# Kernel optimization log

Hardware: AMD Instinct MI355X
Metric: run time of the kernel (lower is better)

The kernel has to match this reference:

```python
import jax, jax.numpy as jnp
import numpy as np

# global prototype index ranges per scale: scale s owns protos [s0, s1)
SCALES = ((0, 100), (100, 200))
NEG = jnp.float32(-1e30)


def _scale_terms(d, lab_flat, cls_of):
    """d: [B,P,Hs,Ws] distances for this scale; lab_flat: [B,N] downsampled labels
    (already shifted by -1); cls_of: [P] class id of each local prototype.
    Returns (sum of exp(-sym_kld) over valid prototype pairs, number of valid pairs).
    """
    B, P = d.shape[0], d.shape[1]
    dflat = d.reshape(B, P, -1)                                   # [B,P,N]
    M = lab_flat[:, None, :] == cls_of[None, :, None]             # [B,P,N] pixel mask per proto's class
    count = M.sum(-1)                                             # [B,P] masked pixel count
    # masked log_softmax over the class pixels of each prototype
    lse = jax.nn.logsumexp(jnp.where(M, dflat, NEG), axis=-1)     # [B,P]
    L = jnp.where(M, dflat - lse[:, :, None], 0.0)                # log-probs on mask, 0 elsewhere
    Pr = jnp.where(M, jnp.exp(L), 0.0)                            # probs on mask, 0 elsewhere
    E = jnp.sum(Pr * L, axis=-1)                                  # [B,P] sum p*log p
    # Cmat[b,a,c] = sum_n Pr[b,a,n] * L[b,c,n]
    Cmat = jnp.einsum('ban,bcn->bac', Pr, L)                      # [B,P,P]
    # sym_kld[b,j,k] = 0.5*((E_k - sum p_k log p_j) + (E_j - sum p_j log p_k))
    kld = 0.5 * (E[:, None, :] + E[:, :, None] - Cmat - jnp.swapaxes(Cmat, 1, 2))
    idx = jnp.arange(P)
    same = (cls_of[:, None] == cls_of[None, :]) & (idx[:, None] < idx[None, :])  # j<k, same class
    valid = same[None] & (count[:, :, None] >= 2) & (count[:, None, :] >= 2)      # need >=2 masked pixels
    return jnp.sum(jnp.where(valid, jnp.exp(-kld), 0.0)), jnp.sum(valid)


def reference(dist0, dist1, target_labels, proto_class):
    lab = target_labels - 1                                       # [B,H,W], -1 = ignore
    B, H, W = lab.shape
    tot = jnp.float32(0.0)
    cnt = jnp.int32(0)
    for d, (s0, s1) in zip((dist0, dist1), SCALES):
        Hs, Ws = d.shape[2], d.shape[3]
        # torch F.interpolate(mode='nearest'): src index = floor(dst * in/out)
        ri = (jnp.arange(Hs) * H) // Hs
        ci = (jnp.arange(Ws) * W) // Ws
        lab_flat = lab[:, ri][:, :, ci].reshape(B, Hs * Ws)
        s, n = _scale_terms(d, lab_flat, proto_class[s0:s1])
        tot = tot + s
        cnt = cnt + n
    return jnp.where(cnt > 0, tot / jnp.maximum(cnt, 1).astype(jnp.float32), jnp.float32(0.0))


def setup_inputs() -> dict:
    key = jax.random.key(0)
    k0, k1, k2 = jax.random.split(key, 3)
    B, C, PPC = 16, 20, 5  # batch, num classes, protos per class per scale
    dist0 = jax.random.normal(k0, (B, 100, 128, 128), dtype=jnp.float32)
    dist1 = jax.random.normal(k1, (B, 100, 64, 64), dtype=jnp.float32)
    # labels in 1..C ; 0 becomes -1 after the shift and is ignored
    target_labels = jax.random.randint(k2, (B, 512, 512), 0, C + 1).astype(jnp.int32)
    proto_class = ((jnp.arange(200) % 100) // PPC).astype(jnp.int32)
    return {"dist0": dist0, "dist1": dist1, "target_labels": target_labels, "proto_class": proto_class}
```

## Files before the change

kernel.cpp:

```cpp
#include <hip/hip_runtime.h>
#include <math.h>

#define TPB 256
#define NCLS 20
#define PPC 5
#define NB 16
#define N0 16384
#define N1 4096
#define SEGCAP 96
#define RECSZ 36
#define NBLKA 1600
#define NBLKB 640

__global__ void downsample_labels(const int* __restrict__ tgt,
                                  char* __restrict__ lab0, char* __restrict__ lab1) {
    const int q = blockIdx.x * blockDim.x + threadIdx.x;
    if (q < 65536) {
        const int b = q >> 12, r = q & 4095;
        const int i = r >> 5, j0 = (r & 31) << 2;
        const int* src = tgt + b * 262144 + (i << 2) * 512;
        char4 v;
        v.x = (char)(src[(j0 + 0) << 2] - 1);
        v.y = (char)(src[(j0 + 1) << 2] - 1);
        v.z = (char)(src[(j0 + 2) << 2] - 1);
        v.w = (char)(src[(j0 + 3) << 2] - 1);
        ((char4*)lab0)[q] = v;
    } else {
        const int k = q - 65536;
        const int b = k >> 10, r = k & 1023;
        const int i = r >> 4, j0 = (r & 15) << 2;
        const int* src = tgt + b * 262144 + (i << 3) * 512;
        char4 v;
        v.x = (char)(src[(j0 + 0) << 3] - 1);
        v.y = (char)(src[(j0 + 1) << 3] - 1);
        v.z = (char)(src[(j0 + 2) << 3] - 1);
        v.w = (char)(src[(j0 + 3) << 3] - 1);
        ((char4*)lab1)[k] = v;
    }
}

__global__ __launch_bounds__(TPB) void kA(const float* __restrict__ dist0,
                                          const float* __restrict__ dist1,
                                          const char* __restrict__ lab0,
                                          const char* __restrict__ lab1,
                                          float* __restrict__ recs) {
    __shared__ float vals[4][PPC][SEGCAP];

    const int blk = blockIdx.x;
    int scale, bc, split;
    if (blk < 1280) { scale = 0; bc = blk >> 2; split = blk & 3; }
    else            { scale = 1; bc = blk - 1280; split = 0; }
    const int b = bc / NCLS, c = bc % NCLS;
    const int N = scale ? N1 : N0;
    const float* dist = scale ? dist1 : dist0;
    const char* lab = (scale ? lab1 + b * N1 : lab0 + b * N0) + split * 4096;

    const float4* rows4[PPC];
#pragma unroll
    for (int p = 0; p < PPC; ++p)
        rows4[p] = (const float4*)(dist + (size_t)(b * 100 + c * PPC + p) * N + split * 4096);
    const char4* lab4 = (const char4*)lab;

    const int tid = threadIdx.x, lane = tid & 63, w = tid >> 6;
    const unsigned long long below = (lane == 63) ? 0x7fffffffffffffffull
                                                  : ((1ull << lane) - 1ull);

    int wK = 0;
#pragma unroll
    for (int it = 0; it < 4; ++it) {
        const int idx4 = w * 256 + it * 64 + lane;
        const char4 lb = lab4[idx4];
        const float4 a0 = rows4[0][idx4], a1 = rows4[1][idx4], a2 = rows4[2][idx4],
                     a3 = rows4[3][idx4], a4 = rows4[4][idx4];
#define DO_E(F)                                                                        \
        { const bool mt = ((int)lb.F == c);                                            \
          const unsigned long long bal = __ballot(mt);                                 \
          if (mt) { const int pos = wK + (int)__popcll(bal & below);                   \
            if (pos < SEGCAP) {                                                        \
              vals[w][0][pos] = a0.F; vals[w][1][pos] = a1.F; vals[w][2][pos] = a2.F;  \
              vals[w][3][pos] = a3.F; vals[w][4][pos] = a4.F; } }                      \
          wK += (int)__popcll(bal); }
        DO_E(x) DO_E(y) DO_E(z) DO_E(w)
#undef DO_E
    }

    float mx[PPC], sm[PPC], T1[PPC * PPC];
#pragma unroll
    for (int p = 0; p < PPC; ++p) { mx[p] = -INFINITY; sm[p] = 0.f; }
#pragma unroll
    for (int i = 0; i < PPC * PPC; ++i) T1[i] = 0.f;

    if (wK <= SEGCAP) {
        for (int k = lane; k < wK; k += 64)
#pragma unroll
            for (int p = 0; p < PPC; ++p) mx[p] = fmaxf(mx[p], vals[w][p][k]);
#pragma unroll
        for (int d = 32; d >= 1; d >>= 1)
#pragma unroll
            for (int p = 0; p < PPC; ++p) mx[p] = fmaxf(mx[p], __shfl_xor(mx[p], d, 64));
        for (int k = lane; k < wK; k += 64) {
            float dv[PPC], ev[PPC];
#pragma unroll
            for (int p = 0; p < PPC; ++p) {
                dv[p] = vals[w][p][k];
                ev[p] = __expf(dv[p] - mx[p]);
                sm[p] += ev[p];
            }
#pragma unroll
            for (int aa = 0; aa < PPC; ++aa)
#pragma unroll
                for (int bb = 0; bb < PPC; ++bb)
                    T1[aa * PPC + bb] = fmaf(ev[aa], dv[bb], T1[aa * PPC + bb]);
        }
    } else {
#pragma unroll
        for (int it = 0; it < 4; ++it) {
            const int idx4 = w * 256 + it * 64 + lane;
            const char4 lb = lab4[idx4];
            const float4 a0 = rows4[0][idx4], a1 = rows4[1][idx4], a2 = rows4[2][idx4],
                         a3 = rows4[3][idx4], a4 = rows4[4][idx4];
#define FB_MAX(F)                                                                      \
            if ((int)lb.F == c) {                                                      \
                mx[0] = fmaxf(mx[0], a0.F); mx[1] = fmaxf(mx[1], a1.F);                \
                mx[2] = fmaxf(mx[2], a2.F); mx[3] = fmaxf(mx[3], a3.F);                \
                mx[4] = fmaxf(mx[4], a4.F); }
            FB_MAX(x) FB_MAX(y) FB_MAX(z) FB_MAX(w)
#undef FB_MAX
        }
#pragma unroll
        for (int d = 32; d >= 1; d >>= 1)
#pragma unroll
            for (int p = 0; p < PPC; ++p) mx[p] = fmaxf(mx[p], __shfl_xor(mx[p], d, 64));
#pragma unroll
        for (int it = 0; it < 4; ++it) {
            const int idx4 = w * 256 + it * 64 + lane;
            const char4 lb = lab4[idx4];
            const float4 a0 = rows4[0][idx4], a1 = rows4[1][idx4], a2 = rows4[2][idx4],
                         a3 = rows4[3][idx4], a4 = rows4[4][idx4];
#define FB_SUM(F)                                                                      \
            if ((int)lb.F == c) {                                                      \
                float dv[PPC] = {a0.F, a1.F, a2.F, a3.F, a4.F};                        \
                float ev[PPC];                                                         \
                _Pragma("unroll")                                                      \
                for (int p = 0; p < PPC; ++p) {                                        \
                    ev[p] = __expf(dv[p] - mx[p]); sm[p] += ev[p]; }                   \
                _Pragma("unroll")                                                      \
                for (int aa = 0; aa < PPC; ++aa)                                       \
                _Pragma("unroll")                                                      \
                    for (int bb = 0; bb < PPC; ++bb)                                   \
                        T1[aa * PPC + bb] = fmaf(ev[aa], dv[bb], T1[aa * PPC + bb]); }
            FB_SUM(x) FB_SUM(y) FB_SUM(z) FB_SUM(w)
#undef FB_SUM
        }
    }

#pragma unroll
    for (int d = 32; d >= 1; d >>= 1) {
#pragma unroll
        for (int p = 0; p < PPC; ++p) sm[p] += __shfl_xor(sm[p], d, 64);
#pragma unroll
        for (int i = 0; i < PPC * PPC; ++i) T1[i] += __shfl_xor(T1[i], d, 64);
    }

    if (lane == 0) {
        float* r = recs + (size_t)(blk * 4 + w) * RECSZ;
#pragma unroll
        for (int p = 0; p < PPC; ++p) { r[p] = mx[p]; r[PPC + p] = sm[p]; }
#pragma unroll
        for (int i = 0; i < PPC * PPC; ++i) r[10 + i] = T1[i];
        r[35] = (float)wK;
    }
}

__global__ __launch_bounds__(64) void kB(const float* __restrict__ recs,
                                         float* __restrict__ psum,
                                         float* __restrict__ pcnt) {
    const int blk = blockIdx.x;
    const int lane = threadIdx.x;
    const int scale = (blk >= 320) ? 1 : 0;
    const int bc = blk - scale * 320;
    const int rbase = scale ? (5120 + bc * 4) : (bc * 16);
    const int nrec = scale ? 4 : 16;
    const int a = (lane < 25) ? lane / 5 : 0;
    const int bb = (lane < 25) ? lane % 5 : 0;

    float M = -INFINITY, cnt = 0.f;
    if (lane < 5)
        for (int r = 0; r < nrec; ++r)
            M = fmaxf(M, recs[(size_t)(rbase + r) * RECSZ + lane]);
    if (lane == 0)
        for (int r = 0; r < nrec; ++r)
            cnt += recs[(size_t)(rbase + r) * RECSZ + 35];
    cnt = __shfl(cnt, 0, 64);

    float S = 0.f;
    if (lane < 5)
        for (int r = 0; r < nrec; ++r) {
            const float* rr = recs + (size_t)(rbase + r) * RECSZ;
            S += rr[5 + lane] * expf(rr[lane] - M);
        }
    float lse = 0.f;
    if (lane < 5) lse = M + logf(S);

    const float Ma    = __shfl(M, a, 64);
    const float Sa    = __shfl(S, a, 64);
    const float lse_b = __shfl(lse, bb, 64);

    float U = 0.f;
    if (lane < 25)
        for (int r = 0; r < nrec; ++r) {
            const float* rr = recs + (size_t)(rbase + r) * RECSZ;
            U += rr[10 + lane] * expf(rr[a] - Ma);
        }
    const float C = U / Sa - lse_b;

    float tot = 0.f;
#pragma unroll
    for (int j = 0; j < PPC; ++j)
#pragma unroll
        for (int k = j + 1; k < PPC; ++k) {
            const float Ejj = __shfl(C, j * 5 + j, 64);
            const float Ekk = __shfl(C, k * 5 + k, 64);
            const float Cjk = __shfl(C, j * 5 + k, 64);
            const float Ckj = __shfl(C, k * 5 + j, 64);
            tot += expf(-0.5f * (Ejj + Ekk - Cjk - Ckj));
        }
    if (lane == 0) {
        const bool ok = (cnt >= 2.f);
        psum[blk] = ok ? tot : 0.f;
        pcnt[blk] = ok ? 10.f : 0.f;
    }
}

__global__ void finalize_kernel(const float* __restrict__ psum,
                                const float* __restrict__ pcnt,
                                float* __restrict__ out) {
    __shared__ float rs[TPB], rc[TPB];
    const int tid = threadIdx.x;
    float s = 0.f, c = 0.f;
    for (int i = tid; i < NBLKB; i += TPB) { s += psum[i]; c += pcnt[i]; }
    rs[tid] = s; rc[tid] = c;
    __syncthreads();
    for (int off = 128; off > 0; off >>= 1) {
        if (tid < off) { rs[tid] += rs[tid + off]; rc[tid] += rc[tid + off]; }
        __syncthreads();
    }
    if (tid == 0) out[0] = (rc[0] > 0.f) ? (rs[0] / rc[0]) : 0.f;
}

extern "C" void kernel_launch(void* const* d_in, const int* in_sizes, int n_in,
                              void* d_out, int out_size, void* d_ws, size_t ws_size,
                              hipStream_t stream) {
    const float* dist0 = (const float*)d_in[0];
    const float* dist1 = (const float*)d_in[1];
    const int*   tgt   = (const int*)d_in[2];
    float* out = (float*)d_out;

    char*  lab0 = (char*)d_ws;
    char*  lab1 = lab0 + 262144;
    float* recs = (float*)(lab0 + 327680);
    float* psum = recs + (size_t)NBLKA * 4 * RECSZ;
    float* pcnt = psum + NBLKB;

    downsample_labels<<<320, TPB, 0, stream>>>(tgt, lab0, lab1);
    kA<<<NBLKA, TPB, 0, stream>>>(dist0, dist1, lab0, lab1, recs);
    kB<<<NBLKB, 64, 0, stream>>>(recs, psum, pcnt);
    finalize_kernel<<<1, TPB, 0, stream>>>(psum, pcnt, out);
}
```

Before: 50.22 us.

## Replace LDS compaction with per-lane online softmax accumulation in kA

Removes the ballot-based compaction into shared memory and the two-pass max/sum (plus the global-reload fallback). Each lane now keeps an online max-rescaled running softmax sum and a 5x5 cross-term matrix over its own masked pixels. The lanes are then merged with a wave-wide max and rescale before the shuffle reductions. All loads are issued up front into registers, and launch bounds request 2 blocks per CU. This trades LDS traffic and the divergent fallback for more exps per masked pixel, heavy register use (80 float4 plus 25 accumulators), and divergent per-lane branches.

```diff
diff --git a/kernel.cpp b/kernel.cpp
--- a/kernel.cpp
+++ b/kernel.cpp
@@ -7,7 +7,6 @@
 #define NB 16
 #define N0 16384
 #define N1 4096
-#define SEGCAP 96
 #define RECSZ 36
 #define NBLKA 1600
 #define NBLKB 640
@@ -39,13 +38,11 @@
     }
 }
 
-__global__ __launch_bounds__(TPB) void kA(const float* __restrict__ dist0,
-                                          const float* __restrict__ dist1,
-                                          const char* __restrict__ lab0,
-                                          const char* __restrict__ lab1,
-                                          float* __restrict__ recs) {
-    __shared__ float vals[4][PPC][SEGCAP];
-
+__global__ __launch_bounds__(TPB, 2) void kA(const float* __restrict__ dist0,
+                                             const float* __restrict__ dist1,
+                                             const char* __restrict__ lab0,
+                                             const char* __restrict__ lab1,
+                                             float* __restrict__ recs) {
     const int blk = blockIdx.x;
     int scale, bc, split;
     if (blk < 1280) { scale = 0; bc = blk >> 2; split = blk & 3; }
@@ -55,120 +52,83 @@
     const float* dist = scale ? dist1 : dist0;
     const char* lab = (scale ? lab1 + b * N1 : lab0 + b * N0) + split * 4096;
 
-    const float4* rows4[PPC];
-#pragma unroll
-    for (int p = 0; p < PPC; ++p)
-        rows4[p] = (const float4*)(dist + (size_t)(b * 100 + c * PPC + p) * N + split * 4096);
+    const int tid = threadIdx.x, lane = tid & 63, w = tid >> 6;
     const char4* lab4 = (const char4*)lab;
-
-    const int tid = threadIdx.x, lane = tid & 63, w = tid >> 6;
-    const unsigned long long below = (lane == 63) ? 0x7fffffffffffffffull
-                                                  : ((1ull << lane) - 1ull);
-
-    int wK = 0;
+    const float* base = dist + (size_t)(b * 100 + c * PPC) * N + split * 4096;
+
+    float4 A[4][PPC];
+    char4 L[4];
 #pragma unroll
     for (int it = 0; it < 4; ++it) {
         const int idx4 = w * 256 + it * 64 + lane;
-        const char4 lb = lab4[idx4];
-        const float4 a0 = rows4[0][idx4], a1 = rows4[1][idx4], a2 = rows4[2][idx4],
-                     a3 = rows4[3][idx4], a4 = rows4[4][idx4];
-#define DO_E(F)                                                                        \
-        { const bool mt = ((int)lb.F == c);                                            \
-          const unsigned long long bal = __ballot(mt);                                 \
-          if (mt) { const int pos = wK + (int)__popcll(bal & below);                   \
-            if (pos < SEGCAP) {                                                        \
-              vals[w][0][pos] = a0.F; vals[w][1][pos] = a1.F; vals[w][2][pos] = a2.F;  \
-              vals[w][3][pos] = a3.F; vals[w][4][pos] = a4.F; } }                      \
-          wK += (int)__popcll(bal); }
+        L[it] = lab4[idx4];
+#pragma unroll
+        for (int p = 0; p < PPC; ++p)
+            A[it][p] = ((const float4*)(base + (size_t)p * N))[idx4];
+    }
+
+    float m[PPC], s[PPC], T1[PPC * PPC];
+#pragma unroll
+    for (int p = 0; p < PPC; ++p) { m[p] = -INFINITY; s[p] = 0.f; }
+#pragma unroll
+    for (int i = 0; i < PPC * PPC; ++i) T1[i] = 0.f;
+    int kcnt = 0;
+
+#pragma unroll
+    for (int it = 0; it < 4; ++it) {
+#define DO_E(F)                                                                     \
+        if ((int)L[it].F == c) {                                                    \
+            float dv[PPC] = {A[it][0].F, A[it][1].F, A[it][2].F,                    \
+                             A[it][3].F, A[it][4].F};                               \
+            _Pragma("unroll")                                                       \
+            for (int p = 0; p < PPC; ++p) {                                         \
+                const float nm = fmaxf(m[p], dv[p]);                                \
+                const float f  = __expf(m[p] - nm);           \
+                const float e  = __expf(dv[p] - nm);                                \
+                m[p] = nm;                                                          \
+                s[p] = s[p] * f + e;                                                \
+                _Pragma("unroll")                                                   \
+                for (int bb = 0; bb < PPC; ++bb)                                    \
+                    T1[p * PPC + bb] = T1[p * PPC + bb] * f + e * dv[bb];           \
+            }                                                                       \
+            ++kcnt;                                                                 \
+        }
         DO_E(x) DO_E(y) DO_E(z) DO_E(w)
 #undef DO_E
     }
 
-    float mx[PPC], sm[PPC], T1[PPC * PPC];
-#pragma unroll
-    for (int p = 0; p < PPC; ++p) { mx[p] = -INFINITY; sm[p] = 0.f; }
-#pragma unroll
-    for (int i = 0; i < PPC * PPC; ++i) T1[i] = 0.f;
-
-    if (wK <= SEGCAP) {
-        for (int k = lane; k < wK; k += 64)
-#pragma unroll
-            for (int p = 0; p < PPC; ++p) mx[p] = fmaxf(mx[p], vals[w][p][k]);
-#pragma unroll
-        for (int d = 32; d >= 1; d >>= 1)
-#pragma unroll
-            for (int p = 0; p < PPC; ++p) mx[p] = fmaxf(mx[p], __shfl_xor(mx[p], d, 64));
-        for (int k = lane; k < wK; k += 64) {
-            float dv[PPC], ev[PPC];
-#pragma unroll
-            for (int p = 0; p < PPC; ++p) {
-                dv[p] = vals[w][p][k];
-                ev[p] = __expf(dv[p] - mx[p]);
-                sm[p] += ev[p];
-            }
-#pragma unroll
-            for (int aa = 0; aa < PPC; ++aa)
-#pragma unroll
-                for (int bb = 0; bb < PPC; ++bb)
-                    T1[aa * PPC + bb] = fmaf(ev[aa], dv[bb], T1[aa * PPC + bb]);
-        }
-    } else {
-#pragma unroll
-        for (int it = 0; it < 4; ++it) {
-            const int idx4 = w * 256 + it * 64 + lane;
-            const char4 lb = lab4[idx4];
-            const float4 a0 = rows4[0][idx4], a1 = rows4[1][idx4], a2 = rows4[2][idx4],
-                         a3 = rows4[3][idx4], a4 = rows4[4][idx4];
-#define FB_MAX(F)                                                                      \
-            if ((int)lb.F == c) {                                                      \
-                mx[0] = fmaxf(mx[0], a0.F); mx[1] = fmaxf(mx[1], a1.F);                \
-                mx[2] = fmaxf(mx[2], a2.F); mx[3] = fmaxf(mx[3], a3.F);                \
-                mx[4] = fmaxf(mx[4], a4.F); }
-            FB_MAX(x) FB_MAX(y) FB_MAX(z) FB_MAX(w)
-#undef FB_MAX
-        }
-#pragma unroll
-        for (int d = 32; d >= 1; d >>= 1)
-#pragma unroll
-            for (int p = 0; p < PPC; ++p) mx[p] = fmaxf(mx[p], __shfl_xor(mx[p], d, 64));
-#pragma unroll
-        for (int it = 0; it < 4; ++it) {
-            const int idx4 = w * 256 + it * 64 + lane;
-            const char4 lb = lab4[idx4];
-            const float4 a0 = rows4[0][idx4], a1 = rows4[1][idx4], a2 = rows4[2][idx4],
-                         a3 = rows4[3][idx4], a4 = rows4[4][idx4];
-#define FB_SUM(F)                                                                      \
-            if ((int)lb.F == c) {                                                      \
-                float dv[PPC] = {a0.F, a1.F, a2.F, a3.F, a4.F};                        \
-                float ev[PPC];                                                         \
-                _Pragma("unroll")                                                      \
-                for (int p = 0; p < PPC; ++p) {                                        \
-                    ev[p] = __expf(dv[p] - mx[p]); sm[p] += ev[p]; }                   \
-                _Pragma("unroll")                                                      \
-                for (int aa = 0; aa < PPC; ++aa)                                       \
-                _Pragma("unroll")                                                      \
-                    for (int bb = 0; bb < PPC; ++bb)                                   \
-                        T1[aa * PPC + bb] = fmaf(ev[aa], dv[bb], T1[aa * PPC + bb]); }
-            FB_SUM(x) FB_SUM(y) FB_SUM(z) FB_SUM(w)
-#undef FB_SUM
-        }
-    }
-
+    float M[PPC];
+#pragma unroll
+    for (int p = 0; p < PPC; ++p) M[p] = m[p];
+#pragma unroll
+    for (int d = 32; d >= 1; d >>= 1)
+#pragma unroll
+        for (int p = 0; p < PPC; ++p) M[p] = fmaxf(M[p], __shfl_xor(M[p], d, 64));
+
+#pragma unroll
+    for (int p = 0; p < PPC; ++p) {
+        const float f = (m[p] == -INFINITY) ? 0.f : __expf(m[p] - M[p]);
+        s[p] *= f;
+#pragma unroll
+        for (int bb = 0; bb < PPC; ++bb) T1[p * PPC + bb] *= f;
+    }
+    float kc = (float)kcnt;
 #pragma unroll
     for (int d = 32; d >= 1; d >>= 1) {
 #pragma unroll
-        for (int p = 0; p < PPC; ++p) sm[p] += __shfl_xor(sm[p], d, 64);
+        for (int p = 0; p < PPC; ++p) s[p] += __shfl_xor(s[p], d, 64);
 #pragma unroll
         for (int i = 0; i < PPC * PPC; ++i) T1[i] += __shfl_xor(T1[i], d, 64);
+        kc += __shfl_xor(kc, d, 64);
     }
 
     if (lane == 0) {
         float* r = recs + (size_t)(blk * 4 + w) * RECSZ;
 #pragma unroll
-        for (int p = 0; p < PPC; ++p) { r[p] = mx[p]; r[PPC + p] = sm[p]; }
+        for (int p = 0; p < PPC; ++p) { r[p] = M[p]; r[PPC + p] = s[p]; }
 #pragma unroll
         for (int i = 0; i < PPC * PPC; ++i) r[10 + i] = T1[i];
-        r[35] = (float)wK;
+        r[35] = kc;
     }
 }
 
```

Result: slower. 51.56 us (+2.7%).
